# Kernel tuning notes

Measured on AMD Instinct MI355X. Metric: run time of the kernel, lower is better.

## Reference

```python
import jax, jax.numpy as jnp
import numpy as np

B, S, D = 1, 2048, 4096
H, HK, HD = 32, 8, 128  # query heads, kv heads, head dim
T_CACHE = 2048
N_REP = H // HK


def setup_inputs() -> dict:
    key = jax.random.key(0)
    ks = jax.random.split(key, 8)
    x = jax.random.normal(ks[0], (B, S, D), dtype=jnp.float32)
    # multiplicative rope factor, broadcast over head axis
    rope = jax.random.uniform(ks[1], (1, S, 1, HD), dtype=jnp.float32, minval=-1.0, maxval=1.0)
    cache_k = jax.random.normal(ks[2], (B, T_CACHE, HK, HD), dtype=jnp.float32)
    cache_v = jax.random.normal(ks[3], (B, T_CACHE, HK, HD), dtype=jnp.float32)
    wq = jax.random.normal(ks[4], (D, H * HD), dtype=jnp.float32) * 0.02
    wk = jax.random.normal(ks[5], (D, HK * HD), dtype=jnp.float32) * 0.02
    wv = jax.random.normal(ks[6], (D, HK * HD), dtype=jnp.float32) * 0.02
    wo = jax.random.normal(ks[7], (H * HD, D), dtype=jnp.float32) * 0.02
    # mask: [1, 1, S, T_CACHE + S]; attend freely to cache, causal within new chunk
    neg = np.float32(-1e9)
    causal = np.triu(np.full((S, S), neg, dtype=np.float32), k=1)
    mask = np.concatenate([np.zeros((S, T_CACHE), dtype=np.float32), causal], axis=1)
    mask = jnp.asarray(mask)[None, None, :, :]
    return {"x": x, "rope": rope, "mask": mask, "cache_k": cache_k,
            "cache_v": cache_v, "wq": wq, "wk": wk, "wv": wv, "wo": wo}


def reference(x, rope, mask, cache_k, cache_v, wq, wk, wv, wo):
    b, s, _ = x.shape
    scale = 1.0 / np.sqrt(HD).astype(np.float32)
    xq = (x @ wq).reshape(b, s, H, HD) * rope          # [b, s, H, hd]
    xk = (x @ wk).reshape(b, s, HK, HD) * rope         # [b, s, HK, hd]
    xv = (x @ wv).reshape(b, s, HK, HD)
    keys = jnp.concatenate([cache_k, xk], axis=1)      # [b, t, HK, hd]
    vals = jnp.concatenate([cache_v, xv], axis=1)
    keys = jnp.repeat(keys, N_REP, axis=2)             # GQA repeat -> [b, t, H, hd]
    vals = jnp.repeat(vals, N_REP, axis=2)
    scores = jnp.einsum('bshd,bthd->bhst', xq, keys) * scale
    scores = scores + mask
    probs = jax.nn.softmax(scores.astype(jnp.float32), axis=-1).astype(xq.dtype)
    out = jnp.einsum('bhst,bthd->bshd', probs, vals).reshape(b, s, H * HD)
    return out @ wo
```

## Files before the change

### kernel.cpp

```cpp
#include <hip/hip_runtime.h>

typedef unsigned short u16;
typedef unsigned int   u32;
typedef short  s16x8 __attribute__((ext_vector_type(8)));
typedef float  f32x4 __attribute__((ext_vector_type(4)));

__device__ __forceinline__ u16 f2bf(float f) {
    union { float f; u32 i; } x; x.f = f;
    u32 r = x.i + 0x7FFFu + ((x.i >> 16) & 1u);
    return (u16)(r >> 16);
}

__device__ __forceinline__ void gld16(const void* g, void* l) {
    __builtin_amdgcn_global_load_lds((const __attribute__((address_space(1))) void*)g,
                                     (__attribute__((address_space(3))) void*)l,
                                     16, 0, 0);
}

__global__ __launch_bounds__(256)
void cast_bf16(const float* __restrict__ in, u16* __restrict__ out, int n4) {
    int g = blockIdx.x * 256 + threadIdx.x;
    if (g >= n4) return;
    float4 v = ((const float4*)in)[g];
    ushort4 o; o.x = f2bf(v.x); o.y = f2bf(v.y); o.z = f2bf(v.z); o.w = f2bf(v.w);
    ((ushort4*)out)[g] = o;
}

__global__ __launch_bounds__(256)
void tconv(const float* __restrict__ B, u16* __restrict__ Bt, int K, int N) {
    __shared__ float T[32][33];
    int n0 = blockIdx.x * 32, k0 = blockIdx.y * 32;
    int t = threadIdx.x;
    int r = t >> 3, c4 = (t & 7) * 4;
    float4 v = *(const float4*)&B[(size_t)(k0 + r) * N + n0 + c4];
    T[r][c4 + 0] = v.x; T[r][c4 + 1] = v.y; T[r][c4 + 2] = v.z; T[r][c4 + 3] = v.w;
    __syncthreads();
    ushort4 o;
    o.x = f2bf(T[c4 + 0][r]); o.y = f2bf(T[c4 + 1][r]);
    o.z = f2bf(T[c4 + 2][r]); o.w = f2bf(T[c4 + 3][r]);
    *(ushort4*)&Bt[(size_t)(n0 + r) * K + k0 + c4] = o;
}

__global__ __launch_bounds__(256)
void kcache_conv(const float* __restrict__ ck, u16* __restrict__ Kc) {
    int g = blockIdx.x * 256 + threadIdx.x;
    int d = (g & 31) * 4, kh = (g >> 5) & 7, t = g >> 8;
    float4 v = *(const float4*)&ck[(size_t)t * 1024 + kh * 128 + d];
    ushort4 o; o.x = f2bf(v.x); o.y = f2bf(v.y); o.z = f2bf(v.z); o.w = f2bf(v.w);
    *(ushort4*)&Kc[(size_t)kh * 524288 + (size_t)t * 128 + d] = o;
}

__global__ __launch_bounds__(256)
void vcache_conv(const float* __restrict__ cv, u16* __restrict__ Vt) {
    __shared__ float T[32][33];
    int t0 = blockIdx.x * 32, d0 = blockIdx.y * 32, kh = blockIdx.z;
    int t = threadIdx.x;
    int r = t >> 3, c4 = (t & 7) * 4;
    float4 v = *(const float4*)&cv[(size_t)(t0 + r) * 1024 + kh * 128 + d0 + c4];
    T[r][c4 + 0] = v.x; T[r][c4 + 1] = v.y; T[r][c4 + 2] = v.z; T[r][c4 + 3] = v.w;
    __syncthreads();
    ushort4 o;
    o.x = f2bf(T[c4 + 0][r]); o.y = f2bf(T[c4 + 1][r]);
    o.z = f2bf(T[c4 + 2][r]); o.w = f2bf(T[c4 + 3][r]);
    *(ushort4*)&Vt[(size_t)(kh * 128 + d0 + r) * 4096 + t0 + c4] = o;
}

__device__ __forceinline__ void gemm_core(const u16* __restrict__ A,
                                          const u16* __restrict__ Bt,
                                          int K, int m0,
                                          u16* As, u16* Bs, f32x4 acc[4][4])
{
    const int tid = threadIdx.x;
    const int lane = tid & 63, w = tid >> 6;
    const int quad = lane >> 4, l15 = lane & 15;
    const int mw = (w >> 1) * 64, nw = (w & 1) * 64;
    const int lrow = tid >> 2;
    const int lcol = ((tid & 3) ^ (lrow & 3)) * 8;
    const int rsw = l15 & 3;

    for (int k0 = 0; k0 < K; k0 += 32) {
        __syncthreads();
        gld16(A  + (size_t)(m0 +      lrow) * K + k0 + lcol, &As[w * 512]);
        gld16(A  + (size_t)(m0 + 64 + lrow) * K + k0 + lcol, &As[2048 + w * 512]);
        gld16(Bt + (size_t)(           lrow) * K + k0 + lcol, &Bs[w * 512]);
        gld16(Bt + (size_t)(      64 + lrow) * K + k0 + lcol, &Bs[2048 + w * 512]);
        __syncthreads();
        s16x8 af[4], bf[4];
        #pragma unroll
        for (int i = 0; i < 4; ++i)
            af[i] = *(const s16x8*)&As[(mw + i * 16 + l15) * 32 + (quad ^ rsw) * 8];
        #pragma unroll
        for (int j = 0; j < 4; ++j)
            bf[j] = *(const s16x8*)&Bs[(nw + j * 16 + l15) * 32 + (quad ^ rsw) * 8];
        #pragma unroll
        for (int i = 0; i < 4; ++i)
            #pragma unroll
            for (int j = 0; j < 4; ++j)
                acc[i][j] = __builtin_amdgcn_mfma_f32_16x16x32_bf16(
                    af[i], bf[j], acc[i][j], 0, 0, 0);
    }
}

__global__ __launch_bounds__(256, 2)
void gemm_qkv(const u16* __restrict__ A, const u16* __restrict__ Wq,
              const u16* __restrict__ Wk, const u16* __restrict__ Wv,
              u16* __restrict__ Qw, u16* __restrict__ Kc, u16* __restrict__ Vt,
              const float* __restrict__ rope)
{
    __shared__ u16 As[128 * 32];
    __shared__ u16 Bs[128 * 32];
    const int m0 = blockIdx.y * 128, n0 = blockIdx.x * 128;

    const u16* Bt;
    if (n0 < 4096)       Bt = Wq + (size_t)n0 * 4096;
    else if (n0 < 5120)  Bt = Wk + (size_t)(n0 - 4096) * 4096;
    else                 Bt = Wv + (size_t)(n0 - 5120) * 4096;

    f32x4 acc[4][4];
    #pragma unroll
    for (int i = 0; i < 4; ++i)
        #pragma unroll
        for (int j = 0; j < 4; ++j) acc[i][j] = (f32x4)0.f;

    gemm_core(A, Bt, 4096, m0, As, Bs, acc);

    const int lane = threadIdx.x & 63, w = threadIdx.x >> 6;
    const int quad = lane >> 4, l15 = lane & 15;
    const int mw = (w >> 1) * 64, nw = (w & 1) * 64;

    #pragma unroll
    for (int i = 0; i < 4; ++i) {
        #pragma unroll
        for (int j = 0; j < 4; ++j) {
            int mm = m0 + mw + i * 16 + quad * 4;
            int nn = n0 + nw + j * 16 + l15;
            if (nn < 4096) {
                #pragma unroll
                for (int r = 0; r < 4; ++r)
                    Qw[(size_t)(mm + r) * 4096 + nn] =
                        f2bf(acc[i][j][r] * rope[(size_t)(mm + r) * 128 + (nn & 127)]
                             * 0.08838834764831845f);
            } else if (nn < 5120) {
                #pragma unroll
                for (int r = 0; r < 4; ++r)
                    Kc[(size_t)((nn - 4096) >> 7) * 524288
                       + (size_t)(2048 + mm + r) * 128 + (nn & 127)] =
                        f2bf(acc[i][j][r] * rope[(size_t)(mm + r) * 128 + (nn & 127)]);
            } else {
                ushort4 o;
                o.x = f2bf(acc[i][j][0]); o.y = f2bf(acc[i][j][1]);
                o.z = f2bf(acc[i][j][2]); o.w = f2bf(acc[i][j][3]);
                *(ushort4*)&Vt[(size_t)(nn - 5120) * 4096 + 2048 + mm] = o;
            }
        }
    }
}

__global__ __launch_bounds__(256, 2)
void gemm_wo(const u16* __restrict__ A, const u16* __restrict__ Bt,
             float* __restrict__ C)
{
    __shared__ u16 As[128 * 32];
    __shared__ u16 Bs[128 * 32];
    const int m0 = blockIdx.y * 128, n0 = blockIdx.x * 128;

    f32x4 acc[4][4];
    #pragma unroll
    for (int i = 0; i < 4; ++i)
        #pragma unroll
        for (int j = 0; j < 4; ++j) acc[i][j] = (f32x4)0.f;

    gemm_core(A, Bt + (size_t)n0 * 4096, 4096, m0, As, Bs, acc);

    const int lane = threadIdx.x & 63, w = threadIdx.x >> 6;
    const int quad = lane >> 4, l15 = lane & 15;
    const int mw = (w >> 1) * 64, nw = (w & 1) * 64;

    #pragma unroll
    for (int i = 0; i < 4; ++i)
        #pragma unroll
        for (int j = 0; j < 4; ++j) {
            int mm = m0 + mw + i * 16 + quad * 4;
            int nn = n0 + nw + j * 16 + l15;
            #pragma unroll
            for (int r = 0; r < 4; ++r)
                C[(size_t)(mm + r) * 4096 + nn] = acc[i][j][r];
        }
}

__global__ __launch_bounds__(256, 2)
void attn_mfma(const u16* __restrict__ Qw, const u16* __restrict__ Kc,
               const u16* __restrict__ Vt, u16* __restrict__ AO)
{
    __shared__ u16 Ks[2][64 * 128];
    __shared__ u16 Vs[2][128 * 64];
    __shared__ u16 Pb[64 * 72];
    __shared__ float Ls[2][64];

    const int tid = threadIdx.x;
    const int lane = tid & 63, w = tid >> 6;
    const int quad = lane >> 4, l15 = lane & 15;
    const int h = blockIdx.x, kh = h >> 2;
    const int q0 = blockIdx.y * 64;
    const int kw = w & 1, qw = w >> 1;
    const size_t kvb = (size_t)kh * 524288;

    s16x8 qreg[2][4];
    #pragma unroll
    for (int n = 0; n < 2; ++n)
        #pragma unroll
        for (int ks = 0; ks < 4; ++ks)
            qreg[n][ks] = *(const s16x8*)&Qw[(size_t)(q0 + qw * 32 + n * 16 + l15) * 4096
                                             + h * 128 + ks * 32 + quad * 8];

    f32x4 o[2][4];
    #pragma unroll
    for (int m = 0; m < 2; ++m)
        #pragma unroll
        for (int n = 0; n < 4; ++n) o[m][n] = (f32x4)0.f;
    float lacc[2] = {0.f, 0.f};

    const int krow = tid >> 4, kcol = ((tid & 15) ^ (krow & 15)) * 8;
    const int vrow = tid >> 3, vcol = ((tid & 7) ^ (vrow & 7)) * 8;
    const int ksw = l15, vsw = l15 & 7;

    const u16* kpg = Kc + kvb + (size_t)krow * 128 + kcol;
    const u16* vpg = Vt + kvb + (size_t)vrow * 4096 + vcol;

    const int kend = 2112 + q0;

    #pragma unroll
    for (int i = 0; i < 4; ++i)
        gld16(kpg + i * 2048, &Ks[0][i * 2048 + w * 512]);
    #pragma unroll
    for (int i = 0; i < 4; ++i)
        gld16(vpg + (size_t)i * 131072, &Vs[0][i * 2048 + w * 512]);

    int cur = 0;
    for (int t0 = 0; t0 < kend; t0 += 64, cur ^= 1) {
        __syncthreads();

        const int t1 = t0 + 64;
        if (t1 < kend) {
            #pragma unroll
            for (int i = 0; i < 4; ++i)
                gld16(kpg + (size_t)t1 * 128 + i * 2048,
                      &Ks[cur ^ 1][i * 2048 + w * 512]);
            #pragma unroll
            for (int i = 0; i < 4; ++i)
                gld16(vpg + (size_t)i * 131072 + t1,
                      &Vs[cur ^ 1][i * 2048 + w * 512]);
        }

        f32x4 sc[2][2];
        sc[0][0] = (f32x4)0.f; sc[0][1] = (f32x4)0.f;
        sc[1][0] = (f32x4)0.f; sc[1][1] = (f32x4)0.f;
        #pragma unroll
        for (int ks = 0; ks < 4; ++ks) {
            int kc8 = (((ks * 4 + quad) ^ ksw) & 15) * 8;
            s16x8 kf0 = *(const s16x8*)&Ks[cur][(kw * 32 +      l15) * 128 + kc8];
            s16x8 kf1 = *(const s16x8*)&Ks[cur][(kw * 32 + 16 + l15) * 128 + kc8];
            sc[0][0] = __builtin_amdgcn_mfma_f32_16x16x32_bf16(kf0, qreg[0][ks], sc[0][0], 0, 0, 0);
            sc[0][1] = __builtin_amdgcn_mfma_f32_16x16x32_bf16(kf0, qreg[1][ks], sc[0][1], 0, 0, 0);
            sc[1][0] = __builtin_amdgcn_mfma_f32_16x16x32_bf16(kf1, qreg[0][ks], sc[1][0], 0, 0, 0);
            sc[1][1] = __builtin_amdgcn_mfma_f32_16x16x32_bf16(kf1, qreg[1][ks], sc[1][1], 0, 0, 0);
        }

        const bool maskt = (t0 + 63 > 2048 + q0);
        #pragma unroll
        for (int m2 = 0; m2 < 2; ++m2) {
            #pragma unroll
            for (int n2 = 0; n2 < 2; ++n2) {
                float e0 = __expf(sc[m2][n2][0]);
                float e1 = __expf(sc[m2][n2][1]);
                float e2 = __expf(sc[m2][n2][2]);
                float e3 = __expf(sc[m2][n2][3]);
                if (maskt) {
                    int key = t0 + kw * 32 + m2 * 16 + quad * 4;
                    int qv  = q0 + qw * 32 + n2 * 16 + l15;
                    if (key + 0 >= 2048 && key + 0 - 2048 > qv) e0 = 0.f;
                    if (key + 1 >= 2048 && key + 1 - 2048 > qv) e1 = 0.f;
                    if (key + 2 >= 2048 && key + 2 - 2048 > qv) e2 = 0.f;
                    if (key + 3 >= 2048 && key + 3 - 2048 > qv) e3 = 0.f;
                }
                lacc[n2] += (e0 + e1) + (e2 + e3);
                uint2 pk;
                pk.x = (u32)f2bf(e0) | ((u32)f2bf(e1) << 16);
                pk.y = (u32)f2bf(e2) | ((u32)f2bf(e3) << 16);
                *(uint2*)&Pb[(qw * 32 + n2 * 16 + l15) * 72 + kw * 32 + m2 * 16 + quad * 4] = pk;
            }
        }

        asm volatile("s_waitcnt lgkmcnt(0)" ::: "memory");
        __builtin_amdgcn_s_barrier();
        asm volatile("" ::: "memory");

        #pragma unroll
        for (int ks = 0; ks < 2; ++ks) {
            int vc8 = (((ks * 4 + quad) ^ vsw) & 7) * 8;
            s16x8 vf0 = *(const s16x8*)&Vs[cur][(w * 32 +      l15) * 64 + vc8];
            s16x8 vf1 = *(const s16x8*)&Vs[cur][(w * 32 + 16 + l15) * 64 + vc8];
            #pragma unroll
            for (int n = 0; n < 4; ++n) {
                s16x8 pf = *(const s16x8*)&Pb[(n * 16 + l15) * 72 + ks * 32 + quad * 8];
                o[0][n] = __builtin_amdgcn_mfma_f32_16x16x32_bf16(vf0, pf, o[0][n], 0, 0, 0);
                o[1][n] = __builtin_amdgcn_mfma_f32_16x16x32_bf16(vf1, pf, o[1][n], 0, 0, 0);
            }
        }
    }

    lacc[0] += __shfl_xor(lacc[0], 16); lacc[0] += __shfl_xor(lacc[0], 32);
    lacc[1] += __shfl_xor(lacc[1], 16); lacc[1] += __shfl_xor(lacc[1], 32);
    if (lane < 16) {
        Ls[kw][qw * 32 +      lane] = lacc[0];
        Ls[kw][qw * 32 + 16 + lane] = lacc[1];
    }
    __syncthreads();

    #pragma unroll
    for (int n = 0; n < 4; ++n) {
        int qq = n * 16 + l15;
        float inv = 1.f / (Ls[0][qq] + Ls[1][qq]);
        #pragma unroll
        for (int m = 0; m < 2; ++m) {
            ushort4 ov;
            ov.x = f2bf(o[m][n][0] * inv);
            ov.y = f2bf(o[m][n][1] * inv);
            ov.z = f2bf(o[m][n][2] * inv);
            ov.w = f2bf(o[m][n][3] * inv);
            *(ushort4*)&AO[(size_t)(q0 + qq) * 4096 + h * 128
                           + w * 32 + m * 16 + quad * 4] = ov;
        }
    }
}

extern "C" void kernel_launch(void* const* d_in, const int* in_sizes, int n_in,
                              void* d_out, int out_size, void* d_ws, size_t ws_size,
                              hipStream_t stream)
{
    const float* x      = (const float*)d_in[0];
    const float* rope   = (const float*)d_in[1];
    const float* cacheK = (const float*)d_in[3];
    const float* cacheV = (const float*)d_in[4];
    const float* wq     = (const float*)d_in[5];
    const float* wk     = (const float*)d_in[6];
    const float* wv     = (const float*)d_in[7];
    const float* wo     = (const float*)d_in[8];
    float* out = (float*)d_out;

    u16* xb = (u16*)d_ws;
    u16* W0 = xb + (size_t)8388608;
    u16* W1 = W0 + (size_t)16777216;
    u16* Qw = W1 + (size_t)4194304;
    u16* Kc = Qw + (size_t)8388608;
    u16* Vt = Kc + (size_t)4194304;
    u16* AO = Vt + (size_t)4194304;
    u16* Wv = AO;

    dim3 blk(256);
    cast_bf16<<<dim3(8192), blk, 0, stream>>>(x, xb, 2097152);
    tconv<<<dim3(128, 128), blk, 0, stream>>>(wq, W0, 4096, 4096);
    tconv<<<dim3(32, 128), blk, 0, stream>>>(wk, W1, 4096, 1024);
    tconv<<<dim3(32, 128), blk, 0, stream>>>(wv, Wv, 4096, 1024);
    gemm_qkv<<<dim3(48, 16), blk, 0, stream>>>(xb, W0, W1, Wv, Qw, Kc, Vt, rope);
    kcache_conv<<<dim3(2048), blk, 0, stream>>>(cacheK, Kc);
    vcache_conv<<<dim3(64, 4, 8), blk, 0, stream>>>(cacheV, Vt);
    attn_mfma<<<dim3(32, 32), blk, 0, stream>>>(Qw, Kc, Vt, AO);
    tconv<<<dim3(128, 128), blk, 0, stream>>>(wo, W0, 4096, 4096);
    gemm_wo<<<dim3(32, 16), blk, 0, stream>>>(AO, W0, out);
}
```

Before: 607.3 us.

## Halve attention KV tile to 32 keys, raise occupancy, and remap blocks by KV head

The attention kernel now processes 32 keys per iteration instead of 64, which halves the LDS used for the K, V and P buffers, and the launch bound is raised to 4 blocks per CU. Block indices are remapped so that consecutive blocks share the same KV head, which should improve L2 reuse of K/V. The V LDS swizzle is redone for the narrower tile. In exchange the loop runs twice as many iterations, each with a barrier, and the register budget tightens.

```diff
diff --git a/kernel.cpp b/kernel.cpp
--- a/kernel.cpp
+++ b/kernel.cpp
@@ -188,20 +188,25 @@
         }
 }
 
-__global__ __launch_bounds__(256, 2)
+__global__ __launch_bounds__(256, 4)
 void attn_mfma(const u16* __restrict__ Qw, const u16* __restrict__ Kc,
                const u16* __restrict__ Vt, u16* __restrict__ AO)
 {
-    __shared__ u16 Ks[2][64 * 128];
-    __shared__ u16 Vs[2][128 * 64];
-    __shared__ u16 Pb[64 * 72];
+    __shared__ u16 Ks[2][32 * 128];
+    __shared__ u16 Vs[2][128 * 32];
+    __shared__ u16 Pb[64 * 40];
     __shared__ float Ls[2][64];
 
     const int tid = threadIdx.x;
     const int lane = tid & 63, w = tid >> 6;
     const int quad = lane >> 4, l15 = lane & 15;
-    const int h = blockIdx.x, kh = h >> 2;
-    const int q0 = blockIdx.y * 64;
+
+    const int bid = blockIdx.x + 32 * blockIdx.y;
+    const int kh = bid & 7;
+    const int inner = bid >> 3;
+    const int h = kh * 4 + (inner & 3);
+    const int q0 = (inner >> 2) * 64;
+
     const int kw = w & 1, qw = w >> 1;
     const size_t kvb = (size_t)kh * 524288;
 
@@ -221,8 +226,7 @@
     float lacc[2] = {0.f, 0.f};
 
     const int krow = tid >> 4, kcol = ((tid & 15) ^ (krow & 15)) * 8;
-    const int vrow = tid >> 3, vcol = ((tid & 7) ^ (vrow & 7)) * 8;
-    const int ksw = l15, vsw = l15 & 7;
+    const int vrow = tid >> 2, vcol = ((tid & 3) ^ ((vrow >> 1) & 3)) * 8;
 
     const u16* kpg = Kc + kvb + (size_t)krow * 128 + kcol;
     const u16* vpg = Vt + kvb + (size_t)vrow * 4096 + vcol;
@@ -230,82 +234,76 @@
     const int kend = 2112 + q0;
 
     #pragma unroll
-    for (int i = 0; i < 4; ++i)
+    for (int i = 0; i < 2; ++i)
         gld16(kpg + i * 2048, &Ks[0][i * 2048 + w * 512]);
     #pragma unroll
-    for (int i = 0; i < 4; ++i)
-        gld16(vpg + (size_t)i * 131072, &Vs[0][i * 2048 + w * 512]);
+    for (int i = 0; i < 2; ++i)
+        gld16(vpg + (size_t)i * 262144, &Vs[0][i * 2048 + w * 512]);
 
     int cur = 0;
-    for (int t0 = 0; t0 < kend; t0 += 64, cur ^= 1) {
+    for (int t0 = 0; t0 < kend; t0 += 32, cur ^= 1) {
         __syncthreads();
 
-        const int t1 = t0 + 64;
+        const int t1 = t0 + 32;
         if (t1 < kend) {
             #pragma unroll
-            for (int i = 0; i < 4; ++i)
+            for (int i = 0; i < 2; ++i)
                 gld16(kpg + (size_t)t1 * 128 + i * 2048,
                       &Ks[cur ^ 1][i * 2048 + w * 512]);
             #pragma unroll
-            for (int i = 0; i < 4; ++i)
-                gld16(vpg + (size_t)i * 131072 + t1,
+            for (int i = 0; i < 2; ++i)
+                gld16(vpg + (size_t)i * 262144 + t1,
                       &Vs[cur ^ 1][i * 2048 + w * 512]);
         }
 
-        f32x4 sc[2][2];
-        sc[0][0] = (f32x4)0.f; sc[0][1] = (f32x4)0.f;
-        sc[1][0] = (f32x4)0.f; sc[1][1] = (f32x4)0.f;
+        f32x4 sc[2];
+        sc[0] = (f32x4)0.f; sc[1] = (f32x4)0.f;
         #pragma unroll
         for (int ks = 0; ks < 4; ++ks) {
-            int kc8 = (((ks * 4 + quad) ^ ksw) & 15) * 8;
-            s16x8 kf0 = *(const s16x8*)&Ks[cur][(kw * 32 +      l15) * 128 + kc8];
-            s16x8 kf1 = *(const s16x8*)&Ks[cur][(kw * 32 + 16 + l15) * 128 + kc8];
-            sc[0][0] = __builtin_amdgcn_mfma_f32_16x16x32_bf16(kf0, qreg[0][ks], sc[0][0], 0, 0, 0);
-            sc[0][1] = __builtin_amdgcn_mfma_f32_16x16x32_bf16(kf0, qreg[1][ks], sc[0][1], 0, 0, 0);
-            sc[1][0] = __builtin_amdgcn_mfma_f32_16x16x32_bf16(kf1, qreg[0][ks], sc[1][0], 0, 0, 0);
-            sc[1][1] = __builtin_amdgcn_mfma_f32_16x16x32_bf16(kf1, qreg[1][ks], sc[1][1], 0, 0, 0);
-        }
-
-        const bool maskt = (t0 + 63 > 2048 + q0);
-        #pragma unroll
-        for (int m2 = 0; m2 < 2; ++m2) {
-            #pragma unroll
-            for (int n2 = 0; n2 < 2; ++n2) {
-                float e0 = __expf(sc[m2][n2][0]);
-                float e1 = __expf(sc[m2][n2][1]);
-                float e2 = __expf(sc[m2][n2][2]);
-                float e3 = __expf(sc[m2][n2][3]);
-                if (maskt) {
-                    int key = t0 + kw * 32 + m2 * 16 + quad * 4;
-                    int qv  = q0 + qw * 32 + n2 * 16 + l15;
-                    if (key + 0 >= 2048 && key + 0 - 2048 > qv) e0 = 0.f;
-                    if (key + 1 >= 2048 && key + 1 - 2048 > qv) e1 = 0.f;
-                    if (key + 2 >= 2048 && key + 2 - 2048 > qv) e2 = 0.f;
-                    if (key + 3 >= 2048 && key + 3 - 2048 > qv) e3 = 0.f;
-                }
-                lacc[n2] += (e0 + e1) + (e2 + e3);
-                uint2 pk;
-                pk.x = (u32)f2bf(e0) | ((u32)f2bf(e1) << 16);
-                pk.y = (u32)f2bf(e2) | ((u32)f2bf(e3) << 16);
-                *(uint2*)&Pb[(qw * 32 + n2 * 16 + l15) * 72 + kw * 32 + m2 * 16 + quad * 4] = pk;
+            int kc8 = (((ks * 4 + quad) ^ l15) & 15) * 8;
+            s16x8 kf = *(const s16x8*)&Ks[cur][(kw * 16 + l15) * 128 + kc8];
+            sc[0] = __builtin_amdgcn_mfma_f32_16x16x32_bf16(kf, qreg[0][ks], sc[0], 0, 0, 0);
+            sc[1] = __builtin_amdgcn_mfma_f32_16x16x32_bf16(kf, qreg[1][ks], sc[1], 0, 0, 0);
+        }
+
+        const bool maskt = (t0 + 31 > 2048 + q0);
+        #pragma unroll
+        for (int n2 = 0; n2 < 2; ++n2) {
+            float e0 = __expf(sc[n2][0]);
+            float e1 = __expf(sc[n2][1]);
+            float e2 = __expf(sc[n2][2]);
+            float e3 = __expf(sc[n2][3]);
+            if (maskt) {
+                int key = t0 + kw * 16 + quad * 4;
+                int qv  = q0 + qw * 32 + n2 * 16 + l15;
+                if (key + 0 >= 2048 && key + 0 - 2048 > qv) e0 = 0.f;
+                if (key + 1 >= 2048 && key + 1 - 2048 > qv) e1 = 0.f;
+                if (key + 2 >= 2048 && key + 2 - 2048 > qv) e2 = 0.f;
+                if (key + 3 >= 2048 && key + 3 - 2048 > qv) e3 = 0.f;
             }
+            lacc[n2] += (e0 + e1) + (e2 + e3);
+            uint2 pk;
+            pk.x = (u32)f2bf(e0) | ((u32)f2bf(e1) << 16);
+            pk.y = (u32)f2bf(e2) | ((u32)f2bf(e3) << 16);
+            *(uint2*)&Pb[(qw * 32 + n2 * 16 + l15) * 40 + kw * 16 + quad * 4] = pk;
         }
 
         asm volatile("s_waitcnt lgkmcnt(0)" ::: "memory");
         __builtin_amdgcn_s_barrier();
         asm volatile("" ::: "memory");
 
-        #pragma unroll
-        for (int ks = 0; ks < 2; ++ks) {
-            int vc8 = (((ks * 4 + quad) ^ vsw) & 7) * 8;
-            s16x8 vf0 = *(const s16x8*)&Vs[cur][(w * 32 +      l15) * 64 + vc8];
-            s16x8 vf1 = *(const s16x8*)&Vs[cur][(w * 32 + 16 + l15) * 64 + vc8];
-            #pragma unroll
-            for (int n = 0; n < 4; ++n) {
-                s16x8 pf = *(const s16x8*)&Pb[(n * 16 + l15) * 72 + ks * 32 + quad * 8];
-                o[0][n] = __builtin_amdgcn_mfma_f32_16x16x32_bf16(vf0, pf, o[0][n], 0, 0, 0);
-                o[1][n] = __builtin_amdgcn_mfma_f32_16x16x32_bf16(vf1, pf, o[1][n], 0, 0, 0);
-            }
+        s16x8 vf[2];
+        #pragma unroll
+        for (int m = 0; m < 2; ++m) {
+            int vr = w * 32 + m * 16 + l15;
+            int vc = (quad ^ ((vr >> 1) & 3)) * 8;
+            vf[m] = *(const s16x8*)&Vs[cur][vr * 32 + vc];
+        }
+        #pragma unroll
+        for (int n = 0; n < 4; ++n) {
+            s16x8 pf = *(const s16x8*)&Pb[(n * 16 + l15) * 40 + quad * 8];
+            o[0][n] = __builtin_amdgcn_mfma_f32_16x16x32_bf16(vf[0], pf, o[0][n], 0, 0, 0);
+            o[1][n] = __builtin_amdgcn_mfma_f32_16x16x32_bf16(vf[1], pf, o[1][n], 0, 0, 0);
         }
     }
 
```

Measured after the change: 601.2 us. About the same (-1.0%).
